# Optimization experiments

Measured on AMD Instinct MI355X. Metric: run time of the kernel, lower is better.

Reference implementation:

```python
import jax, jax.numpy as jnp
import numpy as np

N = 50000      # nodes
E = 400000     # edges (avg degree 8)
G = 64         # graphs in batch
IN_DIM = 128
OUT_DIM = 16


def _linear_params(key, fan_in, fan_out):
    k1, k2 = jax.random.split(key)
    s = 1.0 / np.sqrt(fan_in)
    W = jax.random.uniform(k1, (fan_in, fan_out), minval=-s, maxval=s, dtype=jnp.float32)
    b = jax.random.uniform(k2, (fan_out,), minval=-s, maxval=s, dtype=jnp.float32)
    return W, b


def setup_inputs() -> dict:
    key = jax.random.key(0)
    ks = jax.random.split(key, 12)
    x = jax.random.normal(ks[0], (N, IN_DIM), dtype=jnp.float32)
    edge_index = jax.random.randint(ks[1], (2, E), 0, N)
    # balanced graph assignment (sorted, every graph id present)
    batch = (jnp.arange(N) * G) // N
    W1, b1 = _linear_params(ks[2], IN_DIM, 64)
    W2, b2 = _linear_params(ks[3], 64, 256)
    W3, b3 = _linear_params(ks[4], 256, 512)
    W4, b4 = _linear_params(ks[5], 512, 64)
    Wr, br = _linear_params(ks[6], IN_DIM, 64)
    fc1_W, fc1_b = _linear_params(ks[7], 64, 64)
    fc2_W, fc2_b = _linear_params(ks[8], 64, OUT_DIM)
    ln_g = jnp.ones((64,), jnp.float32); ln_b = jnp.zeros((64,), jnp.float32)
    fcn_g = jnp.ones((64,), jnp.float32); fcn_b = jnp.zeros((64,), jnp.float32)
    return dict(x=x, edge_index=edge_index, batch=batch,
                W1=W1, b1=b1, W2=W2, b2=b2, W3=W3, b3=b3, W4=W4, b4=b4,
                Wr=Wr, br=br, ln_g=ln_g, ln_b=ln_b,
                fc1_W=fc1_W, fc1_b=fc1_b, fcn_g=fcn_g, fcn_b=fcn_b,
                fc2_W=fc2_W, fc2_b=fc2_b)


def _leaky_relu(h):
    return jnp.where(h >= 0, h, 0.01 * h)


def _layer_norm(h, g, b, eps=1e-5):
    m = jnp.mean(h, axis=-1, keepdims=True)
    v = jnp.var(h, axis=-1, keepdims=True)
    return (h - m) * jax.lax.rsqrt(v + eps) * g + b


def reference(x, edge_index, batch, W1, b1, W2, b2, W3, b3, W4, b4,
              Wr, br, ln_g, ln_b, fc1_W, fc1_b, fcn_g, fcn_b, fc2_W, fc2_b):
    src, dst = edge_index[0], edge_index[1]
    n = x.shape[0]
    # PyG GCNConv normalization with self-loops: deg = 1 + in-degree
    deg = jax.ops.segment_sum(jnp.ones(src.shape[0], x.dtype), dst, num_segments=n) + 1.0
    dis = jax.lax.rsqrt(deg)                 # [N]
    edge_norm = (dis[src] * dis[dst])[:, None]   # [E,1]
    self_norm = (dis * dis)[:, None]             # [N,1]

    def gcn_conv(h, W, b):
        h = h @ W                                            # transform first (PyG order)
        agg = jax.ops.segment_sum(h[src] * edge_norm, dst, num_segments=n)
        return agg + h * self_norm + b                       # self-loop term + bias

    residual = x @ Wr + br
    h = _leaky_relu(gcn_conv(x, W1, b1))
    h = _leaky_relu(gcn_conv(h, W2, b2))
    h = _leaky_relu(gcn_conv(h, W3, b3))
    h = _leaky_relu(gcn_conv(h, W4, b4))
    h = _layer_norm(h + residual, ln_g, ln_b)
    # global max pool over graphs
    p = jax.ops.segment_max(h, batch, num_segments=G)        # [G,64]
    p = _layer_norm(p @ fc1_W + fc1_b, fcn_g, fcn_b)
    p = _leaky_relu(p)
    return p @ fc2_W + fc2_b                                 # [G,16]
```

## Files before the change

### kernel.cpp

```cpp
#include <hip/hip_runtime.h>
#include <hip/hip_bf16.h>
#include <math.h>

typedef short bf16x8 __attribute__((ext_vector_type(8)));
typedef short bf16x4 __attribute__((ext_vector_type(4)));
typedef float f32x4 __attribute__((ext_vector_type(4)));

__device__ inline unsigned short f2bf(float f) {
  unsigned u = __float_as_uint(f);
  u += 0x7FFF + ((u >> 16) & 1);
  return (unsigned short)(u >> 16);
}
__device__ inline float bf2f(unsigned short h) {
  return __uint_as_float(((unsigned)h) << 16);
}
__device__ inline float bflo(unsigned u) { return __uint_as_float(u << 16); }
__device__ inline float bfhi(unsigned u) { return __uint_as_float(u & 0xffff0000u); }

__device__ __forceinline__ void gl_lds16(const void* g, void* l) {
  __builtin_amdgcn_global_load_lds((const __attribute__((address_space(1))) void*)g,
                                   (__attribute__((address_space(3))) void*)l, 16, 0, 0);
}


__global__ __launch_bounds__(256) void count_k(const int* __restrict__ dst, int* __restrict__ cnt, int e) {
  int i = blockIdx.x * 256 + threadIdx.x;
  if (i < e) atomicAdd(&cnt[dst[i]], 1);
}

__global__ __launch_bounds__(256) void scan_a(const int* __restrict__ cnt, int* __restrict__ bsum, int n) {
  int i = blockIdx.x * 256 + threadIdx.x;
  int v = (i < n) ? cnt[i] : 0;
#pragma unroll
  for (int o = 32; o > 0; o >>= 1) v += __shfl_xor(v, o);
  __shared__ int ws[4];
  if ((threadIdx.x & 63) == 0) ws[threadIdx.x >> 6] = v;
  __syncthreads();
  if (threadIdx.x == 0) bsum[blockIdx.x] = ws[0] + ws[1] + ws[2] + ws[3];
}

__global__ __launch_bounds__(256) void scan_b(const int* __restrict__ bsum, int* __restrict__ bpre,
                                              int* __restrict__ off_n, int nb) {
  __shared__ int s[256];
  int t = threadIdx.x;
  int v = (t < nb) ? bsum[t] : 0;
  s[t] = v;
  __syncthreads();
  for (int o = 1; o < 256; o <<= 1) {
    int u = (t >= o) ? s[t - o] : 0;
    __syncthreads();
    s[t] += u;
    __syncthreads();
  }
  if (t < nb) bpre[t] = s[t] - v;
  if (t == 255) off_n[0] = s[255];
}

__global__ __launch_bounds__(256) void scan_c(const int* __restrict__ cnt, const int* __restrict__ bpre,
                                              int* __restrict__ off, int* __restrict__ cursor,
                                              float* __restrict__ dis, int n) {
  __shared__ int s[256];
  int i = blockIdx.x * 256 + threadIdx.x;
  int t = threadIdx.x;
  int v = (i < n) ? cnt[i] : 0;
  s[t] = v;
  __syncthreads();
  for (int o = 1; o < 256; o <<= 1) {
    int u = (t >= o) ? s[t - o] : 0;
    __syncthreads();
    s[t] += u;
    __syncthreads();
  }
  if (i < n) {
    int ov = bpre[blockIdx.x] + s[t] - v;
    off[i] = ov;
    cursor[i] = ov;
    dis[i] = rsqrtf((float)v + 1.0f);
  }
}

__global__ __launch_bounds__(256) void scatter_k(const int* __restrict__ src, const int* __restrict__ dst,
                                                 int* __restrict__ cursor, int* __restrict__ csr, int e) {
  int i = blockIdx.x * 256 + threadIdx.x;
  if (i < e) {
    int p = atomicAdd(&cursor[dst[i]], 1);
    csr[p] = src[i];
  }
}


__global__ __launch_bounds__(256) void wconv_k(const float* __restrict__ W1, const float* __restrict__ Wr,
                                               const float* __restrict__ W2, const float* __restrict__ W3,
                                               const float* __restrict__ W4,
                                               short* __restrict__ o1, short* __restrict__ oR,
                                               short* __restrict__ o2, short* __restrict__ o3,
                                               short* __restrict__ o4) {
  int b = blockIdx.x;
  const float* W; short* O; int K, N, nr;
  if (b < 64)       { W = W1; O = o1; K = 128; N = 64;  nr = b; }
  else if (b < 128) { W = Wr; O = oR; K = 128; N = 64;  nr = b - 64; }
  else if (b < 384) { W = W2; O = o2; K = 64;  N = 256; nr = b - 128; }
  else if (b < 896) { W = W3; O = o3; K = 256; N = 512; nr = b - 384; }
  else              { W = W4; O = o4; K = 512; N = 64;  nr = b - 896; }
  for (int k = threadIdx.x; k < K; k += 256)
    O[(size_t)nr * K + k] = (short)f2bf(W[(size_t)k * N + nr]);
}


template<int KT, int NTOT, int WM, int WN, int BIAS, int RELU, int ABF, int OBF, int SPLIT, int SCL, int BLK>
__global__ __launch_bounds__(256, BLK) void mgemm(const void* __restrict__ Av,
                                                  const short* __restrict__ Wc,
                                                  const float* __restrict__ bias,
                                                  void* __restrict__ Cv, void* __restrict__ Cv2,
                                                  const float* __restrict__ scl, int M) {
  __shared__ short As[64 * WM][ABF ? 40 : 72];
  __shared__ short Bs[64 * WN][40];
  const int tid = threadIdx.x;
  const int row0 = blockIdx.x * (64 * WM);
  const int col0 = blockIdx.y * (64 * WN);
  const int w = tid >> 6, lane = tid & 63;
  const int wm = w / WN, wn = w % WN;
  const int rm = wm * 64, cn = wn * 64;
  const int lm = lane & 15, lk = (lane >> 4) * 8;

  f32x4 acc[4][4];
#pragma unroll
  for (int i = 0; i < 4; i++)
#pragma unroll
    for (int j = 0; j < 4; j++)
#pragma unroll
      for (int r = 0; r < 4; r++) acc[i][j][r] = 0.f;

  for (int k0 = 0; k0 < KT; k0 += 32) {
#pragma unroll
    for (int p = 0; p < WM; p++) {
      int r = (tid >> 2) + p * 64;
      int kseg = (tid & 3) * 8;
      int gr = row0 + r;
      if (ABF) {
        bf16x8 v = {0, 0, 0, 0, 0, 0, 0, 0};
        if (gr < M) v = *(const bf16x8*)((const short*)Av + (size_t)gr * KT + k0 + kseg);
        *(bf16x8*)&As[r][kseg] = v;
      } else {
        float4 v0 = {0.f, 0.f, 0.f, 0.f}, v1 = {0.f, 0.f, 0.f, 0.f};
        if (gr < M) {
          const float* ap = (const float*)Av + (size_t)gr * KT + k0 + kseg;
          v0 = *(const float4*)ap;
          v1 = *(const float4*)(ap + 4);
        }
        float vv[8] = {v0.x, v0.y, v0.z, v0.w, v1.x, v1.y, v1.z, v1.w};
        bf16x8 hv, lv;
#pragma unroll
        for (int j = 0; j < 8; j++) {
          unsigned short h = f2bf(vv[j]);
          hv[j] = (short)h;
          lv[j] = (short)f2bf(vv[j] - bf2f(h));
        }
        *(bf16x8*)&As[r][kseg] = hv;
        *(bf16x8*)&As[r][32 + kseg] = lv;
      }
    }
#pragma unroll
    for (int p = 0; p < WN; p++) {
      int nr = (tid >> 2) + p * 64;
      int seg = (tid & 3) * 8;
      *(bf16x8*)&Bs[nr][seg] = *(const bf16x8*)(Wc + (size_t)(col0 + nr) * KT + k0 + seg);
    }
    __syncthreads();

    bf16x8 ah[4], al[4], bb[4];
#pragma unroll
    for (int mt = 0; mt < 4; mt++) {
      ah[mt] = *(const bf16x8*)&As[rm + mt * 16 + lm][lk];
      if (!ABF) al[mt] = *(const bf16x8*)&As[rm + mt * 16 + lm][32 + lk];
    }
#pragma unroll
    for (int nt = 0; nt < 4; nt++) bb[nt] = *(const bf16x8*)&Bs[cn + nt * 16 + lm][lk];
#pragma unroll
    for (int mt = 0; mt < 4; mt++)
#pragma unroll
      for (int nt = 0; nt < 4; nt++) {
        acc[mt][nt] = __builtin_amdgcn_mfma_f32_16x16x32_bf16(ah[mt], bb[nt], acc[mt][nt], 0, 0, 0);
        if (!ABF)
          acc[mt][nt] = __builtin_amdgcn_mfma_f32_16x16x32_bf16(al[mt], bb[nt], acc[mt][nt], 0, 0, 0);
      }
    __syncthreads();
  }

  if (SPLIT) {
    short* epi = (short*)&As[0][0];
    if (wn == 0) {
#pragma unroll
      for (int mt = 0; mt < 4; mt++) {
        int lr = rm + mt * 16 + (lane >> 4) * 4;
#pragma unroll
        for (int r = 0; r < 4; r++) {
          int gr = row0 + lr + r;
          float sc = (SCL && gr < M) ? scl[gr] : 0.f;
#pragma unroll
          for (int nt = 0; nt < 4; nt++)
            epi[(lr + r) * 64 + nt * 16 + lm] = (short)f2bf(acc[mt][nt][r] * sc);
        }
      }
    } else {
#pragma unroll
      for (int mt = 0; mt < 4; mt++) {
        int grb = row0 + rm + mt * 16 + (lane >> 4) * 4;
#pragma unroll
        for (int nt = 0; nt < 4; nt++) {
          int gc = nt * 16 + lm;
          float bv = bias[gc];
#pragma unroll
          for (int r = 0; r < 4; r++) {
            int gr = grb + r;
            if (gr < M) ((float*)Cv2)[(size_t)gr * 64 + gc] = acc[mt][nt][r] + bv;
          }
        }
      }
    }
    __syncthreads();
    int base = tid * 32;
    int row = base >> 6, col = base & 63;
    int gr = row0 + row;
    if (gr < M) {
#pragma unroll
      for (int q = 0; q < 4; q++)
        *(bf16x8*)((short*)Cv + (size_t)gr * 64 + col + q * 8) = *(bf16x8*)&epi[base + q * 8];
    }
  } else if (OBF && WM == 1) {
    short* epi = &Bs[0][0];
    const int NCOL = 64 * WN;
    float bvv[4];
#pragma unroll
    for (int nt = 0; nt < 4; nt++) bvv[nt] = BIAS ? bias[col0 + cn + nt * 16 + lm] : 0.f;
#pragma unroll
    for (int mt = 0; mt < 4; mt++) {
      __syncthreads();
#pragma unroll
      for (int r = 0; r < 4; r++) {
        int gr = row0 + mt * 16 + (lane >> 4) * 4 + r;
        float sc = (SCL && gr < M) ? scl[gr] : 1.f;
#pragma unroll
        for (int nt = 0; nt < 4; nt++) {
          float v = acc[mt][nt][r] + bvv[nt];
          if (RELU) v = (v >= 0.f) ? v : 0.01f * v;
          if (SCL) v *= sc;
          epi[((lane >> 4) * 4 + r) * NCOL + cn + nt * 16 + lm] = (short)f2bf(v);
        }
      }
      __syncthreads();
      const int per = (16 * NCOL) / 256;
      int base = tid * per;
      int lr = base / NCOL, lc = base % NCOL;
      int gr = row0 + mt * 16 + lr;
      if (gr < M) {
#pragma unroll
        for (int q = 0; q < per / 8; q++)
          *(bf16x8*)((short*)Cv + (size_t)gr * NTOT + col0 + lc + q * 8) = *(bf16x8*)&epi[base + q * 8];
      }
    }
  } else {
#pragma unroll
    for (int mt = 0; mt < 4; mt++) {
      int grb = row0 + rm + mt * 16 + (lane >> 4) * 4;
#pragma unroll
      for (int nt = 0; nt < 4; nt++) {
        int gc = col0 + cn + nt * 16 + lm;
        float bv = BIAS ? bias[gc] : 0.f;
#pragma unroll
        for (int r = 0; r < 4; r++) {
          int gr = grb + r;
          if (gr < M) {
            float v = acc[mt][nt][r] + bv;
            if (RELU) v = (v >= 0.f) ? v : 0.01f * v;
            if (SCL) v *= scl[gr];
            if (OBF) ((short*)Cv)[(size_t)gr * NTOT + gc] = (short)f2bf(v);
            else     ((float*)Cv)[(size_t)gr * NTOT + gc] = v;
          }
        }
      }
    }
  }
}


__global__ __launch_bounds__(256, 3) void fused34_k(const short* __restrict__ z3,
                                                    const short* __restrict__ W3c,
                                                    const float* __restrict__ b3,
                                                    const short* __restrict__ W4c,
                                                    const float* __restrict__ dis,
                                                    short* __restrict__ T4, int M) {
  __shared__ __align__(16) char smem[43008];
  short* Bs = (short*)smem;
  const int tid = threadIdx.x;
  const int row0 = blockIdx.x * 64;
  const int w = tid >> 6, lane = tid & 63;
  const int wr = w >> 1, wc = w & 1;
  const int q = lane >> 4, lm = lane & 15;
  short* slab = (short*)(smem + 32768) + w * 1280;

  bf16x8 afr[2][8];
#pragma unroll
  for (int mt = 0; mt < 2; mt++) {
    int gr = row0 + wr * 32 + mt * 16 + lm;
    bool ok = gr < M;
    const short* zp = z3 + (size_t)gr * 256 + q * 8;
#pragma unroll
    for (int k0 = 0; k0 < 8; k0++) {
      bf16x8 v = {0, 0, 0, 0, 0, 0, 0, 0};
      if (ok) v = *(const bf16x8*)(zp + k0 * 32);
      afr[mt][k0] = v;
    }
  }

  f32x4 t4acc[2][4];
#pragma unroll
  for (int mt = 0; mt < 2; mt++)
#pragma unroll
    for (int nt = 0; nt < 4; nt++)
#pragma unroll
      for (int r = 0; r < 4; r++) t4acc[mt][nt][r] = 0.f;

#pragma unroll
  for (int i = 0; i < 4; i++) {
    int seg = w * 4 + i;
    int k0s = seg >> 1, colT = seg & 1;
    const short* gsrc = W3c + (size_t)(colT * 16 + lm) * 256 + k0s * 32 + q * 8;
    gl_lds16(gsrc, Bs + seg * 512);
  }
  __syncthreads();

#pragma unroll
  for (int c = 0; c < 16; c++) {
    const int cur = c & 1, nxt = cur ^ 1;
    if (c < 15) {
#pragma unroll
      for (int i = 0; i < 4; i++) {
        int seg = w * 4 + i;
        int k0s = seg >> 1, colT = seg & 1;
        const short* gsrc = W3c + (size_t)((c + 1) * 32 + colT * 16 + lm) * 256 + k0s * 32 + q * 8;
        gl_lds16(gsrc, Bs + nxt * 8192 + seg * 512);
      }
    }
    float bv = b3[c * 32 + wc * 16 + lm];

    f32x4 acc1[2];
#pragma unroll
    for (int mt = 0; mt < 2; mt++)
#pragma unroll
      for (int r = 0; r < 4; r++) acc1[mt][r] = 0.f;
#pragma unroll
    for (int k0 = 0; k0 < 8; k0++) {
      bf16x8 bb = *(const bf16x8*)(Bs + cur * 8192 + (k0 * 2 + wc) * 512 + lane * 8);
#pragma unroll
      for (int mt = 0; mt < 2; mt++)
        acc1[mt] = __builtin_amdgcn_mfma_f32_16x16x32_bf16(afr[mt][k0], bb, acc1[mt], 0, 0, 0);
    }
#pragma unroll
    for (int mt = 0; mt < 2; mt++)
#pragma unroll
      for (int r = 0; r < 4; r++) {
        float v = acc1[mt][r] + bv;
        v = (v >= 0.f) ? v : 0.01f * v;
        slab[(mt * 16 + q * 4 + r) * 40 + (c & 1) * 16 + lm] = (short)f2bf(v);
      }
    if (c & 1) {
      bf16x8 ha[2];
#pragma unroll
      for (int mt = 0; mt < 2; mt++)
        ha[mt] = *(const bf16x8*)(slab + (mt * 16 + lm) * 40 + q * 8);
      int kb = (c - 1 + (q >> 1)) * 32 + wc * 16 + (q & 1) * 8;
#pragma unroll
      for (int nt = 0; nt < 4; nt++) {
        bf16x8 wb = *(const bf16x8*)(W4c + (size_t)(nt * 16 + lm) * 512 + kb);
#pragma unroll
        for (int mt = 0; mt < 2; mt++)
          t4acc[mt][nt] = __builtin_amdgcn_mfma_f32_16x16x32_bf16(ha[mt], wb, t4acc[mt][nt], 0, 0, 0);
      }
    }
    __syncthreads();
  }

  float* Pf = (float*)smem;
#pragma unroll
  for (int mt = 0; mt < 2; mt++)
#pragma unroll
    for (int nt = 0; nt < 4; nt++)
#pragma unroll
      for (int r = 0; r < 4; r++)
        Pf[wc * 4352 + (size_t)(wr * 32 + mt * 16 + q * 4 + r) * 68 + nt * 16 + lm] = t4acc[mt][nt][r];
  __syncthreads();
  {
    int row = tid >> 2, cb = (tid & 3) * 16;
    int gr = row0 + row;
    if (gr < M) {
      float sc = dis[gr];
      const f32x4* p0 = (const f32x4*)(Pf + (size_t)row * 68 + cb);
      const f32x4* p1 = (const f32x4*)(Pf + 4352 + (size_t)row * 68 + cb);
      bf16x8 o0, o1;
#pragma unroll
      for (int j2 = 0; j2 < 2; j2++) {
        f32x4 s = p0[j2] + p1[j2];
#pragma unroll
        for (int j = 0; j < 4; j++) o0[j2 * 4 + j] = (short)f2bf(s[j] * sc);
      }
#pragma unroll
      for (int j2 = 0; j2 < 2; j2++) {
        f32x4 s = p0[2 + j2] + p1[2 + j2];
#pragma unroll
        for (int j = 0; j < 4; j++) o1[j2 * 4 + j] = (short)f2bf(s[j] * sc);
      }
      *(bf16x8*)(T4 + (size_t)gr * 64 + cb) = o0;
      *(bf16x8*)(T4 + (size_t)gr * 64 + cb + 8) = o1;
    }
  }
}


template<int BR, int OSCL>
__global__ __launch_bounds__(256) void aggb64_k(const short* __restrict__ T, const float* __restrict__ dis,
                                                const int* __restrict__ off, const int* __restrict__ csr,
                                                const float* __restrict__ bias, short* __restrict__ Out, int n) {
  int wv = (blockIdx.x * 256 + threadIdx.x) >> 6;
  int lane = threadIdx.x & 63;
  int qtr = lane >> 4, ql = lane & 15;
  int wid = wv * 4 + qtr;
  if (wid >= n) return;
  float di = dis[wid];
  int e0 = off[wid], e1 = off[wid + 1];
  const uint2* Tw = (const uint2*)T;
  uint2 su = Tw[(size_t)wid * 16 + ql];
  float a0 = bflo(su.x), a1 = bfhi(su.x), a2 = bflo(su.y), a3 = bfhi(su.y);
  int e = e0;
  for (; e + 8 <= e1; e += 8) {
    uint2 u0 = Tw[(size_t)csr[e]     * 16 + ql];
    uint2 u1 = Tw[(size_t)csr[e + 1] * 16 + ql];
    uint2 u2 = Tw[(size_t)csr[e + 2] * 16 + ql];
    uint2 u3 = Tw[(size_t)csr[e + 3] * 16 + ql];
    uint2 u4 = Tw[(size_t)csr[e + 4] * 16 + ql];
    uint2 u5 = Tw[(size_t)csr[e + 5] * 16 + ql];
    uint2 u6 = Tw[(size_t)csr[e + 6] * 16 + ql];
    uint2 u7 = Tw[(size_t)csr[e + 7] * 16 + ql];
    a0 += ((bflo(u0.x) + bflo(u1.x)) + (bflo(u2.x) + bflo(u3.x))) +
          ((bflo(u4.x) + bflo(u5.x)) + (bflo(u6.x) + bflo(u7.x)));
    a1 += ((bfhi(u0.x) + bfhi(u1.x)) + (bfhi(u2.x) + bfhi(u3.x))) +
          ((bfhi(u4.x) + bfhi(u5.x)) + (bfhi(u6.x) + bfhi(u7.x)));
    a2 += ((bflo(u0.y) + bflo(u1.y)) + (bflo(u2.y) + bflo(u3.y))) +
          ((bflo(u4.y) + bflo(u5.y)) + (bflo(u6.y) + bflo(u7.y)));
    a3 += ((bfhi(u0.y) + bfhi(u1.y)) + (bfhi(u2.y) + bfhi(u3.y))) +
          ((bfhi(u4.y) + bfhi(u5.y)) + (bfhi(u6.y) + bfhi(u7.y)));
  }
  for (; e + 4 <= e1; e += 4) {
    uint2 u0 = Tw[(size_t)csr[e]     * 16 + ql];
    uint2 u1 = Tw[(size_t)csr[e + 1] * 16 + ql];
    uint2 u2 = Tw[(size_t)csr[e + 2] * 16 + ql];
    uint2 u3 = Tw[(size_t)csr[e + 3] * 16 + ql];
    a0 += (bflo(u0.x) + bflo(u1.x)) + (bflo(u2.x) + bflo(u3.x));
    a1 += (bfhi(u0.x) + bfhi(u1.x)) + (bfhi(u2.x) + bfhi(u3.x));
    a2 += (bflo(u0.y) + bflo(u1.y)) + (bflo(u2.y) + bflo(u3.y));
    a3 += (bfhi(u0.y) + bfhi(u1.y)) + (bfhi(u2.y) + bfhi(u3.y));
  }
  for (; e < e1; e++) {
    uint2 u = Tw[(size_t)csr[e] * 16 + ql];
    a0 += bflo(u.x); a1 += bfhi(u.x); a2 += bflo(u.y); a3 += bfhi(u.y);
  }
  float v0 = di * a0, v1 = di * a1, v2 = di * a2, v3 = di * a3;
  if (BR) {
    v0 += bias[ql * 4];     v1 += bias[ql * 4 + 1];
    v2 += bias[ql * 4 + 2]; v3 += bias[ql * 4 + 3];
    v0 = (v0 >= 0.f) ? v0 : 0.01f * v0;
    v1 = (v1 >= 0.f) ? v1 : 0.01f * v1;
    v2 = (v2 >= 0.f) ? v2 : 0.01f * v2;
    v3 = (v3 >= 0.f) ? v3 : 0.01f * v3;
  }
  if (OSCL) { v0 *= di; v1 *= di; v2 *= di; v3 *= di; }
  uint2 o;
  o.x = (unsigned)f2bf(v0) | ((unsigned)f2bf(v1) << 16);
  o.y = (unsigned)f2bf(v2) | ((unsigned)f2bf(v3) << 16);
  ((uint2*)Out)[(size_t)wid * 16 + ql] = o;
}

__global__ __launch_bounds__(256) void agg64_ln_k(const short* __restrict__ T, const float* __restrict__ dis,
                                                  const int* __restrict__ off, const int* __restrict__ csr,
                                                  const float* __restrict__ bias, const float* __restrict__ resid,
                                                  const float* __restrict__ g, const float* __restrict__ b,
                                                  float* __restrict__ outh, int n) {
  int wv = (blockIdx.x * 256 + threadIdx.x) >> 6;
  int lane = threadIdx.x & 63;
  int qtr = lane >> 4, ql = lane & 15;
  int wid = wv * 4 + qtr;
  if (wid >= n) return;
  float di = dis[wid];
  int e0 = off[wid], e1 = off[wid + 1];
  const uint2* Tw = (const uint2*)T;
  uint2 su = Tw[(size_t)wid * 16 + ql];
  float a0 = bflo(su.x), a1 = bfhi(su.x), a2 = bflo(su.y), a3 = bfhi(su.y);
  int e = e0;
  for (; e + 8 <= e1; e += 8) {
    uint2 u0 = Tw[(size_t)csr[e]     * 16 + ql];
    uint2 u1 = Tw[(size_t)csr[e + 1] * 16 + ql];
    uint2 u2 = Tw[(size_t)csr[e + 2] * 16 + ql];
    uint2 u3 = Tw[(size_t)csr[e + 3] * 16 + ql];
    uint2 u4 = Tw[(size_t)csr[e + 4] * 16 + ql];
    uint2 u5 = Tw[(size_t)csr[e + 5] * 16 + ql];
    uint2 u6 = Tw[(size_t)csr[e + 6] * 16 + ql];
    uint2 u7 = Tw[(size_t)csr[e + 7] * 16 + ql];
    a0 += ((bflo(u0.x) + bflo(u1.x)) + (bflo(u2.x) + bflo(u3.x))) +
          ((bflo(u4.x) + bflo(u5.x)) + (bflo(u6.x) + bflo(u7.x)));
    a1 += ((bfhi(u0.x) + bfhi(u1.x)) + (bfhi(u2.x) + bfhi(u3.x))) +
          ((bfhi(u4.x) + bfhi(u5.x)) + (bfhi(u6.x) + bfhi(u7.x)));
    a2 += ((bflo(u0.y) + bflo(u1.y)) + (bflo(u2.y) + bflo(u3.y))) +
          ((bflo(u4.y) + bflo(u5.y)) + (bflo(u6.y) + bflo(u7.y)));
    a3 += ((bfhi(u0.y) + bfhi(u1.y)) + (bfhi(u2.y) + bfhi(u3.y))) +
          ((bfhi(u4.y) + bfhi(u5.y)) + (bfhi(u6.y) + bfhi(u7.y)));
  }
  for (; e + 4 <= e1; e += 4) {
    uint2 u0 = Tw[(size_t)csr[e]     * 16 + ql];
    uint2 u1 = Tw[(size_t)csr[e + 1] * 16 + ql];
    uint2 u2 = Tw[(size_t)csr[e + 2] * 16 + ql];
    uint2 u3 = Tw[(size_t)csr[e + 3] * 16 + ql];
    a0 += (bflo(u0.x) + bflo(u1.x)) + (bflo(u2.x) + bflo(u3.x));
    a1 += (bfhi(u0.x) + bfhi(u1.x)) + (bfhi(u2.x) + bfhi(u3.x));
    a2 += (bflo(u0.y) + bflo(u1.y)) + (bflo(u2.y) + bflo(u3.y));
    a3 += (bfhi(u0.y) + bfhi(u1.y)) + (bfhi(u2.y) + bfhi(u3.y));
  }
  for (; e < e1; e++) {
    uint2 u = Tw[(size_t)csr[e] * 16 + ql];
    a0 += bflo(u.x); a1 += bfhi(u.x); a2 += bflo(u.y); a3 += bfhi(u.y);
  }
  float4 rv = ((const float4*)resid)[(size_t)wid * 16 + ql];
  float v0 = di * a0 + bias[ql * 4];
  float v1 = di * a1 + bias[ql * 4 + 1];
  float v2 = di * a2 + bias[ql * 4 + 2];
  float v3 = di * a3 + bias[ql * 4 + 3];
  v0 = (v0 >= 0.f) ? v0 : 0.01f * v0;
  v1 = (v1 >= 0.f) ? v1 : 0.01f * v1;
  v2 = (v2 >= 0.f) ? v2 : 0.01f * v2;
  v3 = (v3 >= 0.f) ? v3 : 0.01f * v3;
  v0 += rv.x; v1 += rv.y; v2 += rv.z; v3 += rv.w;
  float s = (v0 + v1) + (v2 + v3);
  float ss = (v0 * v0 + v1 * v1) + (v2 * v2 + v3 * v3);
#pragma unroll
  for (int o = 8; o > 0; o >>= 1) {
    s += __shfl_xor(s, o);
    ss += __shfl_xor(ss, o);
  }
  float m = s * (1.f / 64.f);
  float var = ss * (1.f / 64.f) - m * m;
  float rs = rsqrtf(var + 1e-5f);
  float4 o4;
  o4.x = (v0 - m) * rs * g[ql * 4]     + b[ql * 4];
  o4.y = (v1 - m) * rs * g[ql * 4 + 1] + b[ql * 4 + 1];
  o4.z = (v2 - m) * rs * g[ql * 4 + 2] + b[ql * 4 + 2];
  o4.w = (v3 - m) * rs * g[ql * 4 + 3] + b[ql * 4 + 3];
  ((float4*)outh)[(size_t)wid * 16 + ql] = o4;
}

__global__ __launch_bounds__(256) void agg256b_k(const short* __restrict__ T, const float* __restrict__ dis,
                                                 const int* __restrict__ off, const int* __restrict__ csr,
                                                 short* __restrict__ Out, int n) {
  int wv = (blockIdx.x * 256 + threadIdx.x) >> 6;
  int lane = threadIdx.x & 63;
  int qtr = lane >> 4, ql = lane & 15;
  int wid = wv * 4 + qtr;
  if (wid >= n) return;
  float di = dis[wid];
  int e0 = off[wid], e1 = off[wid + 1];
  const short* base = T + (size_t)wid * 256 + ql * 16;
  bf16x8 s0 = *(const bf16x8*)base;
  bf16x8 s1 = *(const bf16x8*)(base + 8);
  float a[16];
#pragma unroll
  for (int q = 0; q < 8; q++) { a[q] = bf2f((unsigned short)s0[q]); a[8 + q] = bf2f((unsigned short)s1[q]); }
  int e = e0;
  for (; e + 4 <= e1; e += 4) {
    const short* p0 = T + (size_t)csr[e]     * 256 + ql * 16;
    const short* p1 = T + (size_t)csr[e + 1] * 256 + ql * 16;
    const short* p2 = T + (size_t)csr[e + 2] * 256 + ql * 16;
    const short* p3 = T + (size_t)csr[e + 3] * 256 + ql * 16;
    bf16x8 t00 = *(const bf16x8*)p0, t01 = *(const bf16x8*)(p0 + 8);
    bf16x8 t10 = *(const bf16x8*)p1, t11 = *(const bf16x8*)(p1 + 8);
    bf16x8 t20 = *(const bf16x8*)p2, t21 = *(const bf16x8*)(p2 + 8);
    bf16x8 t30 = *(const bf16x8*)p3, t31 = *(const bf16x8*)(p3 + 8);
#pragma unroll
    for (int q = 0; q < 8; q++) {
      a[q] += (bf2f((unsigned short)t00[q]) + bf2f((unsigned short)t10[q])) +
              (bf2f((unsigned short)t20[q]) + bf2f((unsigned short)t30[q]));
      a[8 + q] += (bf2f((unsigned short)t01[q]) + bf2f((unsigned short)t11[q])) +
                  (bf2f((unsigned short)t21[q]) + bf2f((unsigned short)t31[q]));
    }
  }
  for (; e < e1; e++) {
    const short* p = T + (size_t)csr[e] * 256 + ql * 16;
    bf16x8 t0 = *(const bf16x8*)p, t1 = *(const bf16x8*)(p + 8);
#pragma unroll
    for (int q = 0; q < 8; q++) {
      a[q] += bf2f((unsigned short)t0[q]);
      a[8 + q] += bf2f((unsigned short)t1[q]);
    }
  }
  bf16x8 o0, o1;
#pragma unroll
  for (int q = 0; q < 8; q++) {
    o0[q] = (short)f2bf(di * a[q]);
    o1[q] = (short)f2bf(di * a[8 + q]);
  }
  short* ob = Out + (size_t)wid * 256 + ql * 16;
  *(bf16x8*)ob = o0;
  *(bf16x8*)(ob + 8) = o1;
}


__global__ __launch_bounds__(256) void pool_mlp_k(const float* __restrict__ hn,
                                                  const float* __restrict__ fc1W, const float* __restrict__ fc1b,
                                                  const float* __restrict__ fng, const float* __restrict__ fnb,
                                                  const float* __restrict__ fc2W, const float* __restrict__ fc2b,
                                                  float* __restrict__ out, int n) {
  const int G = 64;
  int g = blockIdx.x;
  int f = threadIdx.x & 63, c = threadIdx.x >> 6;
  long long s0 = ((long long)g * n + G - 1) / G;
  long long e0 = ((long long)(g + 1) * n + G - 1) / G;
  float m = -INFINITY;
  for (long long i = s0 + c; i < e0; i += 4) m = fmaxf(m, hn[(size_t)i * 64 + f]);
  __shared__ float red[4][64];
  __shared__ float ps[64], qs[64];
  red[c][f] = m;
  __syncthreads();
  if (c == 0) ps[f] = fmaxf(fmaxf(red[0][f], red[1][f]), fmaxf(red[2][f], red[3][f]));
  __syncthreads();
  if (threadIdx.x < 64) {
    int lane = threadIdx.x;
    float q = fc1b[lane];
#pragma unroll 8
    for (int k = 0; k < 64; k++) q = fmaf(ps[k], fc1W[k * 64 + lane], q);
    float s = q, ss = q * q;
#pragma unroll
    for (int o = 32; o > 0; o >>= 1) {
      s += __shfl_xor(s, o);
      ss += __shfl_xor(ss, o);
    }
    float mm = s * (1.f / 64.f);
    float var = ss * (1.f / 64.f) - mm * mm;
    float y = (q - mm) * rsqrtf(var + 1e-5f) * fng[lane] + fnb[lane];
    y = (y >= 0.f) ? y : 0.01f * y;
    qs[lane] = y;
    __builtin_amdgcn_wave_barrier();
    if (lane < 16) {
      float o = fc2b[lane];
#pragma unroll 8
      for (int k = 0; k < 64; k++) o = fmaf(qs[k], fc2W[k * 16 + lane], o);
      out[g * 16 + lane] = o;
    }
  }
}


extern "C" void kernel_launch(void* const* d_in, const int* in_sizes, int n_in,
                              void* d_out, int out_size, void* d_ws, size_t ws_size,
                              hipStream_t stream) {
  const float* x   = (const float*)d_in[0];
  const int*   ei  = (const int*)d_in[1];
  const float* W1  = (const float*)d_in[3];
  const float* b1  = (const float*)d_in[4];
  const float* W2  = (const float*)d_in[5];
  const float* b2  = (const float*)d_in[6];
  const float* W3  = (const float*)d_in[7];
  const float* b3  = (const float*)d_in[8];
  const float* W4  = (const float*)d_in[9];
  const float* b4  = (const float*)d_in[10];
  const float* Wr  = (const float*)d_in[11];
  const float* br  = (const float*)d_in[12];
  const float* lng = (const float*)d_in[13];
  const float* lnb = (const float*)d_in[14];
  const float* f1W = (const float*)d_in[15];
  const float* f1b = (const float*)d_in[16];
  const float* fng = (const float*)d_in[17];
  const float* fnb = (const float*)d_in[18];
  const float* f2W = (const float*)d_in[19];
  const float* f2b = (const float*)d_in[20];

  int n = in_sizes[0] / 128;
  int e = in_sizes[1] / 2;
  const int* src = ei;
  const int* dst = ei + e;

  float* arena = (float*)d_ws;
  float* resid = arena;
  short* h2b   = (short*)(arena + (size_t)64 * n);
  short* t4b   = (short*)(arena + (size_t)64 * n);
  short* z3b   = (short*)(arena + (size_t)192 * n);
  float* hn    = arena + (size_t)192 * n;
  short* t1b   = (short*)(arena + (size_t)320 * n);
  short* h1b   = (short*)(arena + (size_t)352 * n);
  short* z2b   = (short*)(arena + (size_t)384 * n);
  float* dis   = arena + (size_t)448 * n;
  int* cnt    = (int*)(dis + n);
  int* off    = cnt + n;
  int* cursor = off + n + 1;
  int* csr    = cursor + n;
  int* bsum   = csr + e;
  int* bpre   = bsum + 256;
  float* pool = (float*)(bpre + 256);
  size_t wq = (((size_t)(pool + 4096)) + 15) & ~(size_t)15;
  short* wc1 = (short*)wq;
  short* wcR = wc1 + 8192;
  short* wc2 = wcR + 8192;
  short* wc3 = wc2 + 16384;
  short* wc4 = wc3 + 131072;
  size_t need = ((char*)(wc4 + 32768) - (char*)d_ws) + 64;
  if (ws_size < need) return;

  int nb_n = (n + 255) / 256;
  int nb_e = (e + 255) / 256;
  int nb_w4 = ((n + 3) / 4 + 3) / 4;
  int g_wide = (n + 63) / 64;
  int g_fused = (n + 127) / 128;

  wconv_k<<<960, 256, 0, stream>>>(W1, Wr, W2, W3, W4, wc1, wcR, wc2, wc3, wc4);

  hipMemsetAsync(cnt, 0, (size_t)n * sizeof(int), stream);
  count_k<<<nb_e, 256, 0, stream>>>(dst, cnt, e);
  scan_a<<<nb_n, 256, 0, stream>>>(cnt, bsum, n);
  scan_b<<<1, 256, 0, stream>>>(bsum, bpre, off + n, nb_n);
  scan_c<<<nb_n, 256, 0, stream>>>(cnt, bpre, off, cursor, dis, n);
  scatter_k<<<nb_e, 256, 0, stream>>>(src, dst, cursor, csr, e);

  mgemm<128, 128, 2, 2, 1, 0, 0, 0, 1, 1, 4><<<dim3(g_fused, 1), 256, 0, stream>>>(x, wc1, br, t1b, resid, dis, n);
  aggb64_k<1, 1><<<nb_w4, 256, 0, stream>>>(t1b, dis, off, csr, b1, h1b, n);
  aggb64_k<0, 0><<<nb_w4, 256, 0, stream>>>(h1b, dis, off, csr, nullptr, z2b, n);
  mgemm<64, 256, 1, 4, 1, 1, 1, 1, 0, 1, 5><<<dim3(g_wide, 1), 256, 0, stream>>>(z2b, wc2, b2, h2b, nullptr, dis, n);
  agg256b_k<<<nb_w4, 256, 0, stream>>>(h2b, dis, off, csr, z3b, n);
  fused34_k<<<g_wide, 256, 0, stream>>>(z3b, wc3, b3, wc4, dis, t4b, n);
  agg64_ln_k<<<nb_w4, 256, 0, stream>>>(t4b, dis, off, csr, b4, resid, lng, lnb, hn, n);
  pool_mlp_k<<<64, 256, 0, stream>>>(hn, f1W, f1b, fng, fnb, f2W, f2b, (float*)d_out, n);
}
```

Measured before the change: 366.6 us.

## Stage W3/W4 tiles through registers into LDS and do the second GEMM every chunk

Drops the global_load_lds async copies of W3 tiles. W3 and W4 chunks are now prefetched into registers and written to double-buffered LDS after compute, and W4 is staged in LDS instead of being read straight from global memory. The second MFMA stage now runs every chunk, zero-masking the A operand by lane group, rather than every other chunk from a shared 32-wide slab. This removes the uncoalesced global W4 reads at the cost of more LDS (49 KB, which may hurt occupancy at 3 blocks/CU), extra register pressure, and redundant MFMAs on zeroed operands.

After: 358.0 us. 2.3% less time.

```diff
diff --git a/kernel.cpp b/kernel.cpp
--- a/kernel.cpp
+++ b/kernel.cpp
@@ -16,11 +16,6 @@
 }
 __device__ inline float bflo(unsigned u) { return __uint_as_float(u << 16); }
 __device__ inline float bfhi(unsigned u) { return __uint_as_float(u & 0xffff0000u); }
-
-__device__ __forceinline__ void gl_lds16(const void* g, void* l) {
-  __builtin_amdgcn_global_load_lds((const __attribute__((address_space(1))) void*)g,
-                                   (__attribute__((address_space(3))) void*)l, 16, 0, 0);
-}
 
 
 __global__ __launch_bounds__(256) void count_k(const int* __restrict__ dst, int* __restrict__ cnt, int e) {
@@ -290,21 +285,23 @@
                                                     const short* __restrict__ W4c,
                                                     const float* __restrict__ dis,
                                                     short* __restrict__ T4, int M) {
-  __shared__ __align__(16) char smem[43008];
-  short* Bs = (short*)smem;
+  __shared__ __align__(16) char smem[49152];
+  short* Bs  = (short*)smem;
+  short* Ws4 = (short*)(smem + 32768);
   const int tid = threadIdx.x;
   const int row0 = blockIdx.x * 64;
   const int w = tid >> 6, lane = tid & 63;
   const int wr = w >> 1, wc = w & 1;
   const int q = lane >> 4, lm = lane & 15;
-  short* slab = (short*)(smem + 32768) + w * 1280;
+  const int lk = q * 8;
+  short* slab = (short*)(smem + 43008) + w * 768;
 
   bf16x8 afr[2][8];
 #pragma unroll
   for (int mt = 0; mt < 2; mt++) {
     int gr = row0 + wr * 32 + mt * 16 + lm;
     bool ok = gr < M;
-    const short* zp = z3 + (size_t)gr * 256 + q * 8;
+    const short* zp = z3 + (size_t)gr * 256 + lk;
 #pragma unroll
     for (int k0 = 0; k0 < 8; k0++) {
       bf16x8 v = {0, 0, 0, 0, 0, 0, 0, 0};
@@ -321,28 +318,27 @@
 #pragma unroll
       for (int r = 0; r < 4; r++) t4acc[mt][nt][r] = 0.f;
 
-#pragma unroll
-  for (int i = 0; i < 4; i++) {
-    int seg = w * 4 + i;
-    int k0s = seg >> 1, colT = seg & 1;
-    const short* gsrc = W3c + (size_t)(colT * 16 + lm) * 256 + k0s * 32 + q * 8;
-    gl_lds16(gsrc, Bs + seg * 512);
-  }
+  const short* w3base = W3c + (size_t)(wc * 16 + lm) * 256 + wr * 32 + lk;
+  const int w4row = tid >> 2, w4seg = (tid & 3) * 8;
+
+  bf16x8 pw3[4];
+  bf16x8 pw4;
+#pragma unroll
+  for (int q4 = 0; q4 < 4; q4++) pw3[q4] = *(const bf16x8*)(w3base + q4 * 64);
+  pw4 = *(const bf16x8*)(W4c + (size_t)w4row * 512 + w4seg);
+#pragma unroll
+  for (int q4 = 0; q4 < 4; q4++) *(bf16x8*)&Bs[q4 * 2048 + tid * 8] = pw3[q4];
+  *(bf16x8*)&Ws4[(size_t)w4row * 40 + w4seg] = pw4;
   __syncthreads();
 
-#pragma unroll
   for (int c = 0; c < 16; c++) {
-    const int cur = c & 1, nxt = cur ^ 1;
+    int cur = c & 1, nxt = cur ^ 1;
     if (c < 15) {
 #pragma unroll
-      for (int i = 0; i < 4; i++) {
-        int seg = w * 4 + i;
-        int k0s = seg >> 1, colT = seg & 1;
-        const short* gsrc = W3c + (size_t)((c + 1) * 32 + colT * 16 + lm) * 256 + k0s * 32 + q * 8;
-        gl_lds16(gsrc, Bs + nxt * 8192 + seg * 512);
-      }
-    }
-    float bv = b3[c * 32 + wc * 16 + lm];
+      for (int q4 = 0; q4 < 4; q4++)
+        pw3[q4] = *(const bf16x8*)(w3base + (size_t)(c + 1) * 8192 + q4 * 64);
+      pw4 = *(const bf16x8*)(W4c + (size_t)w4row * 512 + (c + 1) * 32 + w4seg);
+    }
 
     f32x4 acc1[2];
 #pragma unroll
@@ -351,32 +347,40 @@
       for (int r = 0; r < 4; r++) acc1[mt][r] = 0.f;
 #pragma unroll
     for (int k0 = 0; k0 < 8; k0++) {
-      bf16x8 bb = *(const bf16x8*)(Bs + cur * 8192 + (k0 * 2 + wc) * 512 + lane * 8);
+      bf16x8 bb = *(const bf16x8*)&Bs[cur * 8192 + (k0 * 2 + wc) * 512 + lane * 8];
 #pragma unroll
       for (int mt = 0; mt < 2; mt++)
         acc1[mt] = __builtin_amdgcn_mfma_f32_16x16x32_bf16(afr[mt][k0], bb, acc1[mt], 0, 0, 0);
     }
+    float bv = b3[c * 32 + wc * 16 + lm];
 #pragma unroll
     for (int mt = 0; mt < 2; mt++)
 #pragma unroll
       for (int r = 0; r < 4; r++) {
         float v = acc1[mt][r] + bv;
         v = (v >= 0.f) ? v : 0.01f * v;
-        slab[(mt * 16 + q * 4 + r) * 40 + (c & 1) * 16 + lm] = (short)f2bf(v);
-      }
-    if (c & 1) {
-      bf16x8 ha[2];
-#pragma unroll
-      for (int mt = 0; mt < 2; mt++)
-        ha[mt] = *(const bf16x8*)(slab + (mt * 16 + lm) * 40 + q * 8);
-      int kb = (c - 1 + (q >> 1)) * 32 + wc * 16 + (q & 1) * 8;
-#pragma unroll
-      for (int nt = 0; nt < 4; nt++) {
-        bf16x8 wb = *(const bf16x8*)(W4c + (size_t)(nt * 16 + lm) * 512 + kb);
-#pragma unroll
-        for (int mt = 0; mt < 2; mt++)
-          t4acc[mt][nt] = __builtin_amdgcn_mfma_f32_16x16x32_bf16(ha[mt], wb, t4acc[mt][nt], 0, 0, 0);
-      }
+        slab[(mt * 16 + q * 4 + r) * 24 + lm] = (short)f2bf(v);
+      }
+    {
+      bool act = (q >> 1) == wc;
+      bf16x8 bb2[4];
+#pragma unroll
+      for (int nt = 0; nt < 4; nt++)
+        bb2[nt] = *(const bf16x8*)&Ws4[(size_t)cur * 2560 + (nt * 16 + lm) * 40 + lk];
+#pragma unroll
+      for (int mt = 0; mt < 2; mt++) {
+        bf16x8 hv = *(const bf16x8*)&slab[(mt * 16 + lm) * 24 + (q & 1) * 8];
+        if (!act) hv = (bf16x8){0, 0, 0, 0, 0, 0, 0, 0};
+#pragma unroll
+        for (int nt = 0; nt < 4; nt++)
+          t4acc[mt][nt] = __builtin_amdgcn_mfma_f32_16x16x32_bf16(hv, bb2[nt], t4acc[mt][nt], 0, 0, 0);
+      }
+    }
+    if (c < 15) {
+#pragma unroll
+      for (int q4 = 0; q4 < 4; q4++)
+        *(bf16x8*)&Bs[nxt * 8192 + q4 * 2048 + tid * 8] = pw3[q4];
+      *(bf16x8*)&Ws4[(size_t)nxt * 2560 + (size_t)w4row * 40 + w4seg] = pw4;
     }
     __syncthreads();
   }
```
